# Performance work log

Measured on AMD Instinct MI355X. Metric: run time of the kernel, lower is better.

Reference implementation:

```python
import jax, jax.numpy as jnp
import numpy as np

B, N, E_PER = 64, 1024, 32768
IN_DIM, HID, K = 128, 128, 64
EPS = 1e-15


def setup_inputs() -> dict:
    key = jax.random.key(0)
    ks = jax.random.split(key, 16)
    x = jax.random.normal(ks[0], (B * N, IN_DIM), jnp.float32)
    off = (jnp.arange(B, dtype=jnp.int32) * N)[:, None]
    src = (jax.random.randint(ks[1], (B, E_PER), 0, N, dtype=jnp.int32) + off).reshape(-1)
    dst = (jax.random.randint(ks[2], (B, E_PER), 0, N, dtype=jnp.int32) + off).reshape(-1)
    edge_index = jnp.stack([src, dst])
    batch = jnp.repeat(jnp.arange(B, dtype=jnp.int32), N)

    def lin(k, i, o):
        return (jax.random.normal(k, (i, o), jnp.float32) / np.sqrt(i)).astype(jnp.float32)

    params = dict(
        W1l=lin(ks[3], IN_DIM, HID), b1l=jnp.zeros((HID,), jnp.float32), W1r=lin(ks[4], IN_DIM, HID),
        W2l=lin(ks[5], HID, K), b2l=jnp.zeros((K,), jnp.float32), W2r=lin(ks[6], HID, K),
        Wm=lin(ks[7], K, K), bm=jnp.zeros((K,), jnp.float32),
        Wrel=lin(ks[8], HID, HID), Wroot=lin(ks[9], HID, HID), broot=jnp.zeros((HID,), jnp.float32),
        Wc1=lin(ks[10], HID * K, HID), bc1=jnp.zeros((HID,), jnp.float32),
        Wc2=lin(ks[11], HID, 1), bc2=jnp.zeros((1,), jnp.float32),
    )
    return dict(x=x, edge_index=edge_index, batch=batch, num_graphs=B, nodes_per_graph=N, **params)


def _sage(x, src, dst, Wl, bl, Wr, n):
    # PyG SAGEConv: lin_l(mean_{j in N(i)} x_j) + lin_r(x_i); lin_r has no bias.
    agg = jax.ops.segment_sum(x[src], dst, num_segments=n)
    deg = jax.ops.segment_sum(jnp.ones((src.shape[0],), x.dtype), dst, num_segments=n)
    agg = agg / jnp.maximum(deg, 1.0)[:, None]
    return agg @ Wl + bl + x @ Wr


def reference(x, edge_index, batch, num_graphs, nodes_per_graph,
              W1l, b1l, W1r, W2l, b2l, W2r, Wm, bm,
              Wrel, Wroot, broot, Wc1, bc1, Wc2, bc2):
    Bn, Nn = num_graphs, nodes_per_graph
    n_total = Bn * Nn
    src, dst = edge_index[0], edge_index[1]

    z = jax.nn.leaky_relu(_sage(x, src, dst, W1l, b1l, W1r, n_total), 0.01)
    s = jax.nn.leaky_relu(_sage(z, src, dst, W2l, b2l, W2r, n_total), 0.01)
    s = s @ Wm + bm

    # to_dense_batch (equal-size graphs -> mask all True) and to_dense_adj
    z = z.reshape(Bn, Nn, -1)                      # [B, N, HID]
    s = s.reshape(Bn, Nn, -1)                      # [B, N, K]
    a = jnp.zeros((Bn, Nn, Nn), x.dtype).at[src // Nn, src % Nn, dst % Nn].add(1.0)

    # dense_diff_pool
    s = jax.nn.softmax(s, axis=-1)
    pooled = jnp.einsum('bnk,bnf->bkf', s, z)      # [B, K, HID]
    adj_p = jnp.einsum('bnk,bnm,bml->bkl', s, a, s)  # [B, K, K]
    link_loss = jnp.sqrt(jnp.sum((a - jnp.einsum('bnk,bmk->bnm', s, s)) ** 2)) / a.size
    ent_loss = jnp.mean(jnp.sum(-s * jnp.log(s + EPS), axis=-1))

    # DenseSAGEConv: lin_rel(adj@x / deg) + lin_root(x)
    agg = jnp.matmul(adj_p, pooled) / jnp.maximum(adj_p.sum(-1, keepdims=True), 1.0)
    h = jax.nn.leaky_relu(agg @ Wrel + pooled @ Wroot + broot, 0.01)

    h = h.reshape(Bn, -1)                          # [B, K*HID]
    logits = (jax.nn.leaky_relu(h @ Wc1 + bc1, 0.01) @ Wc2 + bc2).squeeze(-1)
    return logits, link_loss + ent_loss
```

## Files before the change

### kernel.cpp

```cpp
#include <hip/hip_runtime.h>
#include <math.h>

#define BATCH 64
#define NPG 1024
#define NT (BATCH*NPG)
#define EPER 32768
#define ETOT (BATCH*EPER)

typedef __attribute__((ext_vector_type(4))) float f32x4;
typedef __attribute__((ext_vector_type(8))) short s16x8;

__device__ __forceinline__ float lky(float x){ return x > 0.f ? x : 0.01f*x; }
__device__ __forceinline__ unsigned short f2bf(float f){
    unsigned u = __float_as_uint(f);
    u = u + 0x7FFFu + ((u >> 16) & 1u);
    return (unsigned short)(u >> 16);
}
__device__ __forceinline__ float bf2f_lo(unsigned v){ return __uint_as_float(v << 16); }
__device__ __forceinline__ float bf2f_hi(unsigned v){ return __uint_as_float(v & 0xFFFF0000u); }

__global__ void k_castx(const float* __restrict__ in, unsigned short* __restrict__ out, int n4){
    int i = blockIdx.x*256 + threadIdx.x;
    if (i < n4){
        float4 v = ((const float4*)in)[i];
        ushort4 o = { f2bf(v.x), f2bf(v.y), f2bf(v.z), f2bf(v.w) };
        ((ushort4*)out)[i] = o;
    }
}

__global__ void k_wprep(const float* __restrict__ W1l, const float* __restrict__ W1r,
                        const float* __restrict__ W2l, const float* __restrict__ W2r,
                        unsigned short* __restrict__ wt){
    int i = blockIdx.x*256 + threadIdx.x;
    if (i < 16384){ int k = i >> 7, n = i & 127; wt[n*128 + k] = f2bf(W1l[i]); }
    else if (i < 32768){ int j = i - 16384; int k = j >> 7, n = j & 127; wt[16384 + n*128 + k] = f2bf(W1r[j]); }
    else if (i < 40960){ int j = i - 32768; int k = j >> 6, n = j & 63; wt[32768 + n*128 + k] = f2bf(W2l[j]); }
    else if (i < 49152){ int j = i - 40960; int k = j >> 6, n = j & 63; wt[40960 + n*128 + k] = f2bf(W2r[j]); }
}

__global__ void __launch_bounds__(1024) k_a2lds(const int* __restrict__ src, const int* __restrict__ dst,
                                                unsigned* __restrict__ acc_out){
    __shared__ unsigned nib[32768];
    __shared__ unsigned red[16];
    int b = blockIdx.x, pass = blockIdx.y, tid = threadIdx.x;
    for (int i = tid; i < 32768; i += 1024) nib[i] = 0;
    __syncthreads();
    int base = b*EPER;
    for (int i = tid; i < EPER; i += 1024){
        unsigned key = (((unsigned)src[base+i] & 1023u) << 10) | ((unsigned)dst[base+i] & 1023u);
        if ((int)(key >> 18) == pass)
            atomicAdd(&nib[(key & 0x3FFFFu) >> 3], 1u << ((key & 7u)*4u));
    }
    __syncthreads();
    unsigned local = 0;
    for (int i = tid; i < 32768; i += 1024){
        unsigned w = nib[i];
        if (w){
            #pragma unroll
            for (int q = 0; q < 8; q++){ unsigned c = (w >> (4*q)) & 15u; local += c*c; }
        }
    }
    for (int o = 32; o; o >>= 1) local += __shfl_xor(local, o);
    if ((tid & 63) == 0) red[tid >> 6] = local;
    __syncthreads();
    if (tid == 0){
        unsigned s = 0;
        for (int q = 0; q < 16; q++) s += red[q];
        atomicAdd(acc_out, s);
    }
}

__global__ void __launch_bounds__(1024) k_csr(const int* __restrict__ src, const int* __restrict__ dst,
                                              int* __restrict__ ipd, int* __restrict__ ips,
                                              unsigned short* __restrict__ lst_d,
                                              unsigned short* __restrict__ lst_s){
    __shared__ unsigned eds[EPER];
    __shared__ int cnt[1024];
    __shared__ int buf[1024];
    int g = blockIdx.x, which = blockIdx.y, tid = threadIdx.x;
    cnt[tid] = 0;
    __syncthreads();
    int base = g*EPER;
    for (int i = tid; i < EPER; i += 1024){
        unsigned s = (unsigned)src[base+i] & 1023u;
        unsigned d = (unsigned)dst[base+i] & 1023u;
        eds[i] = (s << 10) | d;
        atomicAdd(&cnt[which ? s : d], 1);
    }
    __syncthreads();
    int v = cnt[tid];
    int x = v;
    buf[tid] = x; __syncthreads();
    for (int off = 1; off < 1024; off <<= 1){
        int t = (tid >= off) ? buf[tid - off] : 0;
        __syncthreads();
        x += t; buf[tid] = x; __syncthreads();
    }
    int excl = x - v;
    int* ip = which ? ips : ipd;
    ip[g*1024 + tid] = base + excl;
    if (g == 0 && tid == 0) ip[NT] = ETOT;
    cnt[tid] = excl;
    __syncthreads();
    unsigned short* lst = which ? lst_s : lst_d;
    for (int i = tid; i < EPER; i += 1024){
        unsigned key = eds[i];
        unsigned d = key & 1023u, s = key >> 10;
        unsigned idx = which ? s : d;
        unsigned val = which ? d : s;
        int p = atomicAdd(&cnt[idx], 1);
        lst[base + p] = (unsigned short)val;
    }
}

template<int MODE, int TD>
__global__ void __launch_bounds__(1024) k_aggl(
        const unsigned short* __restrict__ X, const int* __restrict__ indptr,
        const unsigned short* __restrict__ lst,
        const unsigned short* __restrict__ R, const float* __restrict__ bias,
        unsigned short* __restrict__ out){
    __shared__ uint2 tab[1024*9];
    constexpr int PPG = (TD == 128) ? 8 : 4;
    int bid = blockIdx.x;
    int xcd = bid & 7, j = bid >> 3;
    int gi = j / PPG, part = j - gi*PPG;
    int graph = xcd + 8*gi;
    int fpart = part >> 1;
    int npart = part & 1;
    int foff = fpart*32;
    int nbase_loc = npart*512;
    int tid = threadIdx.x;
    int gb = graph*NPG;
    for (int i = tid; i < 8192; i += 1024){
        int row = i >> 3, q = i & 7;
        tab[row*9 + q] = *(const uint2*)&X[(size_t)(gb+row)*TD + foff + q*4];
    }
    __syncthreads();
    int g = tid & 7;
    for (int c = 0; c < 4; c++){
        int node = gb + nbase_loc + c*128 + (tid >> 3);
        int st = indptr[node], en = indptr[node+1];
        float a0 = 0.f, a1 = 0.f, a2 = 0.f, a3 = 0.f;
        int e = st;
        for (; e + 4 <= en; e += 4){
            int r0 = lst[e+0], r1 = lst[e+1], r2 = lst[e+2], r3 = lst[e+3];
            uint2 v0 = tab[r0*9 + g];
            uint2 v1 = tab[r1*9 + g];
            uint2 v2 = tab[r2*9 + g];
            uint2 v3 = tab[r3*9 + g];
            a0 += bf2f_lo(v0.x) + bf2f_lo(v1.x) + bf2f_lo(v2.x) + bf2f_lo(v3.x);
            a1 += bf2f_hi(v0.x) + bf2f_hi(v1.x) + bf2f_hi(v2.x) + bf2f_hi(v3.x);
            a2 += bf2f_lo(v0.y) + bf2f_lo(v1.y) + bf2f_lo(v2.y) + bf2f_lo(v3.y);
            a3 += bf2f_hi(v0.y) + bf2f_hi(v1.y) + bf2f_hi(v2.y) + bf2f_hi(v3.y);
        }
        for (; e < en; e++){
            uint2 v = tab[lst[e]*9 + g];
            a0 += bf2f_lo(v.x); a1 += bf2f_hi(v.x);
            a2 += bf2f_lo(v.y); a3 += bf2f_hi(v.y);
        }
        if (MODE >= 1){
            int dg = en - st;
            float inv = 1.f/(float)(dg > 1 ? dg : 1);
            a0 *= inv; a1 *= inv; a2 *= inv; a3 *= inv;
        }
        if (MODE == 2){
            uint2 r = *(const uint2*)&R[(size_t)node*TD + foff + 4*g];
            a0 = lky(a0 + bf2f_lo(r.x) + bias[foff + 4*g + 0]);
            a1 = lky(a1 + bf2f_hi(r.x) + bias[foff + 4*g + 1]);
            a2 = lky(a2 + bf2f_lo(r.y) + bias[foff + 4*g + 2]);
            a3 = lky(a3 + bf2f_hi(r.y) + bias[foff + 4*g + 3]);
        }
        uint2 pk;
        pk.x = (unsigned)f2bf(a0) | ((unsigned)f2bf(a1) << 16);
        pk.y = (unsigned)f2bf(a2) | ((unsigned)f2bf(a3) << 16);
        *(uint2*)&out[(size_t)node*TD + foff + 4*g] = pk;
    }
}

template<int N>
__global__ void __launch_bounds__(512) k_mfma2b(
        const unsigned short* __restrict__ Ah, const unsigned short* __restrict__ Wt1,
        const unsigned short* __restrict__ Wt2, unsigned short* __restrict__ C1,
        unsigned short* __restrict__ C2){
    __shared__ unsigned short ldsB[2*N*128];
    int tid = threadIdx.x;
    for (int i = tid; i < N*64; i += 512){
        int n = i >> 6, kk = i & 63;
        int swz = (n*256 + 4*kk) ^ ((n & 7) << 4);
        *(unsigned*)((char*)ldsB + swz)         = ((const unsigned*)Wt1)[i];
        *(unsigned*)((char*)ldsB + N*256 + swz) = ((const unsigned*)Wt2)[i];
    }
    __syncthreads();
    int wave = tid >> 6, l = tid & 63;
    int lr = l & 15, lg = l >> 4;
    constexpr int NF = N/16;
    int arow = blockIdx.x*128 + wave*16 + lr;
    f32x4 acc1[NF], acc2[NF];
    f32x4 zv = {0.f, 0.f, 0.f, 0.f};
    #pragma unroll
    for (int nf = 0; nf < NF; nf++){ acc1[nf] = zv; acc2[nf] = zv; }
    #pragma unroll
    for (int ks = 0; ks < 4; ks++){
        s16x8 af = *(const s16x8*)(Ah + (size_t)arow*128 + ks*32 + lg*8);
        #pragma unroll
        for (int nf = 0; nf < NF; nf++){
            int n = nf*16 + lr;
            int swz = (n*256 + ks*64 + lg*16) ^ ((n & 7) << 4);
            s16x8 b1 = *(const s16x8*)((const char*)ldsB + swz);
            s16x8 b2 = *(const s16x8*)((const char*)ldsB + N*256 + swz);
            acc1[nf] = __builtin_amdgcn_mfma_f32_16x16x32_bf16(af, b1, acc1[nf], 0, 0, 0);
            acc2[nf] = __builtin_amdgcn_mfma_f32_16x16x32_bf16(af, b2, acc2[nf], 0, 0, 0);
        }
    }
    int orow = blockIdx.x*128 + wave*16 + lg*4;
    #pragma unroll
    for (int nf = 0; nf < NF; nf++){
        int c = nf*16 + lr;
        #pragma unroll
        for (int j = 0; j < 4; j++){
            size_t idx = (size_t)(orow + j)*N + c;
            C1[idx] = f2bf(acc1[nf][j]);
            C2[idx] = f2bf(acc2[nf][j]);
        }
    }
}

__global__ void __launch_bounds__(256) k_gemm(
        const float* __restrict__ A1, const float* __restrict__ A2,
        const float* __restrict__ W1, const float* __restrict__ W2,
        const float* __restrict__ bias, void* __restrict__ C,
        int M, int Nn, int Kd, int dual, int act, int obf){
    __shared__ float sA1[16*68], sB1[16*68], sA2[16*68], sB2[16*68];
    int tid = threadIdx.x;
    int m0 = blockIdx.x*64, n0 = blockIdx.y*64;
    int tx = tid & 15, ty = tid >> 4;
    int lr = tid >> 2, lk = (tid & 3)*4;
    int wk = tid >> 4, wn = (tid & 15)*4;
    float acc[4][4] = {};
    for (int k0 = 0; k0 < Kd; k0 += 16){
        float4 a1 = *(const float4*)&A1[(size_t)(m0+lr)*Kd + k0 + lk];
        float4 w1 = *(const float4*)&W1[(size_t)(k0+wk)*Nn + n0 + wn];
        sA1[(lk+0)*68+lr] = a1.x; sA1[(lk+1)*68+lr] = a1.y;
        sA1[(lk+2)*68+lr] = a1.z; sA1[(lk+3)*68+lr] = a1.w;
        *(float4*)&sB1[wk*68+wn] = w1;
        if (dual){
            float4 a2 = *(const float4*)&A2[(size_t)(m0+lr)*Kd + k0 + lk];
            float4 w2 = *(const float4*)&W2[(size_t)(k0+wk)*Nn + n0 + wn];
            sA2[(lk+0)*68+lr] = a2.x; sA2[(lk+1)*68+lr] = a2.y;
            sA2[(lk+2)*68+lr] = a2.z; sA2[(lk+3)*68+lr] = a2.w;
            *(float4*)&sB2[wk*68+wn] = w2;
        }
        __syncthreads();
        #pragma unroll
        for (int kk = 0; kk < 16; kk++){
            float4 av = *(const float4*)&sA1[kk*68 + ty*4];
            float4 bv = *(const float4*)&sB1[kk*68 + tx*4];
            float a[4] = {av.x, av.y, av.z, av.w};
            float b[4] = {bv.x, bv.y, bv.z, bv.w};
            #pragma unroll
            for (int i = 0; i < 4; i++)
                #pragma unroll
                for (int j = 0; j < 4; j++) acc[i][j] += a[i]*b[j];
            if (dual){
                float4 av2 = *(const float4*)&sA2[kk*68 + ty*4];
                float4 bv2 = *(const float4*)&sB2[kk*68 + tx*4];
                float a2[4] = {av2.x, av2.y, av2.z, av2.w};
                float b2[4] = {bv2.x, bv2.y, bv2.z, bv2.w};
                #pragma unroll
                for (int i = 0; i < 4; i++)
                    #pragma unroll
                    for (int j = 0; j < 4; j++) acc[i][j] += a2[i]*b2[j];
            }
        }
        __syncthreads();
    }
    float bb[4] = {0.f, 0.f, 0.f, 0.f};
    if (bias){
        #pragma unroll
        for (int j = 0; j < 4; j++) bb[j] = bias[n0 + tx*4 + j];
    }
    #pragma unroll
    for (int i = 0; i < 4; i++){
        float v0 = acc[i][0]+bb[0], v1 = acc[i][1]+bb[1], v2 = acc[i][2]+bb[2], v3 = acc[i][3]+bb[3];
        if (act){ v0 = lky(v0); v1 = lky(v1); v2 = lky(v2); v3 = lky(v3); }
        size_t idx = (size_t)(m0 + ty*4 + i)*Nn + n0 + tx*4;
        if (obf){
            ushort4 o = { f2bf(v0), f2bf(v1), f2bf(v2), f2bf(v3) };
            *(ushort4*)&((unsigned short*)C)[idx] = o;
        } else {
            float4 o = { v0, v1, v2, v3 };
            *(float4*)&((float*)C)[idx] = o;
        }
    }
}

__global__ void __launch_bounds__(256) k_gemm_wm(
        const unsigned short* __restrict__ agg2h, const unsigned short* __restrict__ r2h,
        const float* __restrict__ b2l, const float* __restrict__ Wm,
        const float* __restrict__ bm,
        unsigned short* __restrict__ Sh, float* __restrict__ ent_acc){
    __shared__ float sA[16*68], sB[16*68];
    __shared__ float red[256];
    int tid = threadIdx.x;
    int m0 = blockIdx.x*64;
    int tx = tid & 15, ty = tid >> 4;
    int lr = tid >> 2, lk = (tid & 3)*4;
    int wk = tid >> 4, wn = (tid & 15)*4;
    float acc[4][4] = {};
    for (int k0 = 0; k0 < 64; k0 += 16){
        uint2 a = *(const uint2*)&agg2h[(size_t)(m0+lr)*64 + k0 + lk];
        uint2 r = *(const uint2*)&r2h[(size_t)(m0+lr)*64 + k0 + lk];
        sA[(lk+0)*68+lr] = lky(bf2f_lo(a.x) + bf2f_lo(r.x) + b2l[k0+lk+0]);
        sA[(lk+1)*68+lr] = lky(bf2f_hi(a.x) + bf2f_hi(r.x) + b2l[k0+lk+1]);
        sA[(lk+2)*68+lr] = lky(bf2f_lo(a.y) + bf2f_lo(r.y) + b2l[k0+lk+2]);
        sA[(lk+3)*68+lr] = lky(bf2f_hi(a.y) + bf2f_hi(r.y) + b2l[k0+lk+3]);
        *(float4*)&sB[wk*68+wn] = *(const float4*)&Wm[(size_t)(k0+wk)*64 + wn];
        __syncthreads();
        #pragma unroll
        for (int kk = 0; kk < 16; kk++){
            float4 av = *(const float4*)&sA[kk*68 + ty*4];
            float4 bv = *(const float4*)&sB[kk*68 + tx*4];
            float a4[4] = {av.x, av.y, av.z, av.w};
            float b4[4] = {bv.x, bv.y, bv.z, bv.w};
            #pragma unroll
            for (int i = 0; i < 4; i++)
                #pragma unroll
                for (int j = 0; j < 4; j++) acc[i][j] += a4[i]*b4[j];
        }
        __syncthreads();
    }
    float bb[4];
    #pragma unroll
    for (int j = 0; j < 4; j++) bb[j] = bm[tx*4 + j];
    float ent_local = 0.f;
    #pragma unroll
    for (int i = 0; i < 4; i++){
        float v[4];
        #pragma unroll
        for (int j = 0; j < 4; j++) v[j] = acc[i][j] + bb[j];
        float m = fmaxf(fmaxf(v[0], v[1]), fmaxf(v[2], v[3]));
        for (int o = 1; o < 16; o <<= 1) m = fmaxf(m, __shfl_xor(m, o));
        float e[4];
        float sm = 0.f;
        #pragma unroll
        for (int j = 0; j < 4; j++){ e[j] = __expf(v[j] - m); sm += e[j]; }
        for (int o = 1; o < 16; o <<= 1) sm += __shfl_xor(sm, o);
        float inv = 1.f/sm;
        float p[4];
        float w = 0.f;
        #pragma unroll
        for (int j = 0; j < 4; j++){
            p[j] = e[j]*inv;
            w += -p[j]*__logf(p[j] + 1e-15f);
        }
        for (int o = 1; o < 16; o <<= 1) w += __shfl_xor(w, o);
        if (tx == 0) ent_local += w;
        size_t idx = (size_t)(m0 + ty*4 + i)*64 + tx*4;
        ushort4 oh = { f2bf(p[0]), f2bf(p[1]), f2bf(p[2]), f2bf(p[3]) };
        *(ushort4*)&Sh[idx] = oh;
    }
    red[tid] = ent_local; __syncthreads();
    for (int o = 128; o; o >>= 1){ if (tid < o) red[tid] += red[tid+o]; __syncthreads(); }
    if (tid == 0) atomicAdd(ent_acc, red[0]);
}

__global__ void __launch_bounds__(1024) k_spmm(
        const unsigned short* __restrict__ Sh, const unsigned short* __restrict__ Zh,
        const unsigned short* __restrict__ Th, float* __restrict__ pbuf){
    __shared__ unsigned short At[64*72];
    __shared__ unsigned short Bt[256*72];
    int bid = blockIdx.x;
    int xcd = bid & 7, j = bid >> 3;
    int graph = xcd + 8*(j & 7);
    int kp = j >> 3;
    int tid = threadIdx.x;
    int w = tid >> 6, l = tid & 63;
    int lr = l & 15, lg = l >> 4;
    int mt = w & 3, ng = w >> 2;
    f32x4 acc[4];
    f32x4 zv = {0.f, 0.f, 0.f, 0.f};
    #pragma unroll
    for (int q = 0; q < 4; q++) acc[q] = zv;
    int gb = graph*NPG;
    int sa_n = tid & 63, sa_c = (tid >> 6)*4;
    int sb_k = tid & 63, sb_g = tid >> 6;
    for (int n0 = kp*256; n0 < kp*256 + 256; n0 += 64){
        ushort4 sv = *(const ushort4*)&Sh[(size_t)(gb+n0+sa_n)*64 + sa_c];
        At[(sa_c+0)*72 + sa_n] = sv.x;
        At[(sa_c+1)*72 + sa_n] = sv.y;
        At[(sa_c+2)*72 + sa_n] = sv.z;
        At[(sa_c+3)*72 + sa_n] = sv.w;
        {
            int R = gb + n0 + sb_k;
            const unsigned short* srcp;
            if (sb_g < 8)       srcp = &Zh[(size_t)R*128 + sb_g*16];
            else if (sb_g < 12) srcp = &Th[(size_t)R*64 + (sb_g-8)*16];
            else                srcp = &Sh[(size_t)R*64 + (sb_g-12)*16];
            ushort4 a0 = *(const ushort4*)(srcp);
            ushort4 a1 = *(const ushort4*)(srcp+4);
            ushort4 a2 = *(const ushort4*)(srcp+8);
            ushort4 a3 = *(const ushort4*)(srcp+12);
            int cb = sb_g*16;
            Bt[(cb+ 0)*72+sb_k]=a0.x; Bt[(cb+ 1)*72+sb_k]=a0.y; Bt[(cb+ 2)*72+sb_k]=a0.z; Bt[(cb+ 3)*72+sb_k]=a0.w;
            Bt[(cb+ 4)*72+sb_k]=a1.x; Bt[(cb+ 5)*72+sb_k]=a1.y; Bt[(cb+ 6)*72+sb_k]=a1.z; Bt[(cb+ 7)*72+sb_k]=a1.w;
            Bt[(cb+ 8)*72+sb_k]=a2.x; Bt[(cb+ 9)*72+sb_k]=a2.y; Bt[(cb+10)*72+sb_k]=a2.z; Bt[(cb+11)*72+sb_k]=a2.w;
            Bt[(cb+12)*72+sb_k]=a3.x; Bt[(cb+13)*72+sb_k]=a3.y; Bt[(cb+14)*72+sb_k]=a3.z; Bt[(cb+15)*72+sb_k]=a3.w;
        }
        __syncthreads();
        #pragma unroll
        for (int ks = 0; ks < 2; ks++){
            s16x8 af = *(const s16x8*)&At[(mt*16+lr)*72 + ks*32 + lg*8];
            #pragma unroll
            for (int q = 0; q < 4; q++){
                s16x8 bf = *(const s16x8*)&Bt[((ng*4+q)*16+lr)*72 + ks*32 + lg*8];
                acc[q] = __builtin_amdgcn_mfma_f32_16x16x32_bf16(af, bf, acc[q], 0, 0, 0);
            }
        }
        __syncthreads();
    }
    float* pb = pbuf + ((size_t)graph*4 + kp)*16384;
    #pragma unroll
    for (int q = 0; q < 4; q++){
        int col = (ng*4+q)*16 + lr;
        #pragma unroll
        for (int j2 = 0; j2 < 4; j2++){
            int m = mt*16 + lg*4 + j2;
            pb[m*256 + col] = acc[q][j2];
        }
    }
}

__global__ void k_spmmred(const float* __restrict__ pbuf,
                          float* __restrict__ P, float* __restrict__ AP,
                          float* __restrict__ GR,
                          float* __restrict__ redt, float* __restrict__ reds){
    int i = blockIdx.x*256 + threadIdx.x;
    int g = i >> 14;
    int r = i & 16383;
    int m = r >> 8, col = r & 255;
    const float* pb = pbuf + (size_t)g*65536 + r;
    float v = pb[0] + pb[16384] + pb[32768] + pb[49152];
    float tr = 0.f, sq = 0.f;
    if (col < 128){
        P[((size_t)g*64 + m)*128 + col] = v;
    } else if (col < 192){
        AP[((size_t)g*64 + m)*64 + (col-128)] = v;
        if (col-128 == m) tr = v;
    } else {
        GR[((size_t)g*64 + m)*64 + (col-192)] = v;
        sq = v*v;
    }
    for (int o = 32; o; o >>= 1){ tr += __shfl_xor(tr, o); sq += __shfl_xor(sq, o); }
    __shared__ float rt[4], rs[4];
    if ((threadIdx.x & 63) == 0){ rt[threadIdx.x >> 6] = tr; rs[threadIdx.x >> 6] = sq; }
    __syncthreads();
    if (threadIdx.x == 0){
        redt[blockIdx.x] = rt[0]+rt[1]+rt[2]+rt[3];
        reds[blockIdx.x] = rs[0]+rs[1]+rs[2]+rs[3];
    }
}

__global__ void __launch_bounds__(1024) k_redfin(const float* __restrict__ redt,
                                                 const float* __restrict__ reds,
                                                 float* __restrict__ crossp,
                                                 float* __restrict__ normgp){
    int tid = threadIdx.x;
    float t = redt[tid] + redt[tid+1024] + redt[tid+2048] + redt[tid+3072];
    float s = reds[tid] + reds[tid+1024] + reds[tid+2048] + reds[tid+3072];
    for (int o = 32; o; o >>= 1){ t += __shfl_xor(t, o); s += __shfl_xor(s, o); }
    __shared__ float rt[16], rs[16];
    if ((tid & 63) == 0){ rt[tid >> 6] = t; rs[tid >> 6] = s; }
    __syncthreads();
    if (tid == 0){
        float st = 0.f, ss = 0.f;
        for (int q = 0; q < 16; q++){ st += rt[q]; ss += rs[q]; }
        atomicAdd(crossp, st);
        atomicAdd(normgp, ss);
    }
}

__global__ void __launch_bounds__(256) k_heada(
        const float* __restrict__ AP, const float* __restrict__ P,
        float* __restrict__ aggout){
    __shared__ float sapT[64*65];
    __shared__ float sp[64*33];
    __shared__ float srs[64];
    int b = blockIdx.x, c0 = blockIdx.y*32;
    int tid = threadIdx.x;
    for (int i = tid; i < 4096; i += 256){
        int k = i >> 6, l = i & 63;
        sapT[l*65 + k] = AP[(size_t)b*4096 + i];
    }
    for (int i = tid; i < 2048; i += 256){
        int l = i >> 5, j = i & 31;
        sp[l*33 + j] = P[(size_t)b*8192 + l*128 + c0 + j];
    }
    __syncthreads();
    if (tid < 64){
        float s = 0.f;
        for (int l = 0; l < 64; l++) s += sapT[l*65 + tid];
        srs[tid] = fmaxf(s, 1.f);
    }
    __syncthreads();
    int k = tid & 63, jg = (tid >> 6)*8;
    float acc[8] = {};
    for (int l = 0; l < 64; l++){
        float a = sapT[l*65 + k];
        #pragma unroll
        for (int j = 0; j < 8; j++) acc[j] += a*sp[l*33 + jg + j];
    }
    float inv = 1.f/srs[k];
    #pragma unroll
    for (int j = 0; j < 8; j++)
        aggout[(size_t)b*8192 + k*128 + c0 + jg + j] = acc[j]*inv;
}

__global__ void __launch_bounds__(256) k_head2(
        const float* __restrict__ hbuf, const float* __restrict__ Wc1,
        float* __restrict__ hcacc){
    __shared__ float sh[512];
    __shared__ float sred[256];
    int b = blockIdx.x >> 4, ch = blockIdx.x & 15;
    int tid = threadIdx.x;
    for (int i = tid; i < 512; i += 256) sh[i] = hbuf[(size_t)b*8192 + ch*512 + i];
    __syncthreads();
    int j = tid & 127, half = tid >> 7;
    float acc = 0.f;
    const float* W = Wc1 + (size_t)(ch*512 + half*256)*128;
    const float* hh = sh + half*256;
    for (int r = 0; r < 256; r++) acc += hh[r]*W[(size_t)r*128 + j];
    sred[tid] = acc; __syncthreads();
    if (tid < 128) atomicAdd(&hcacc[(size_t)b*128 + tid], sred[tid] + sred[tid+128]);
}

__global__ void k_head3(const float* __restrict__ hcacc, const float* __restrict__ bc1,
                        const float* __restrict__ Wc2, const float* __restrict__ bc2,
                        float* __restrict__ out){
    int b = blockIdx.x, t = threadIdx.x;
    float hc = lky(hcacc[(size_t)b*128 + t] + bc1[t]);
    float p = hc*Wc2[t];
    for (int o = 32; o; o >>= 1) p += __shfl_xor(p, o);
    __shared__ float r2[2];
    if ((t & 63) == 0) r2[t >> 6] = p;
    __syncthreads();
    if (t == 0) out[b] = r2[0] + r2[1] + bc2[0];
}

__global__ void k_finalize(const unsigned int* __restrict__ a2,
                           const float* __restrict__ cross,
                           const float* __restrict__ normg,
                           const float* __restrict__ ent,
                           float* __restrict__ out){
    float ss = (float)(*a2) - 2.f*(*cross) + (*normg);
    if (ss < 0.f) ss = 0.f;
    float link = sqrtf(ss) / 67108864.f;
    out[64] = link + (*ent)/(float)NT;
}

extern "C" void kernel_launch(void* const* d_in, const int* in_sizes, int n_in,
                              void* d_out, int out_size, void* d_ws, size_t ws_size,
                              hipStream_t stream){
    const float* x    = (const float*)d_in[0];
    const int*   ei   = (const int*)d_in[1];
    const int*   src  = ei;
    const int*   dst  = ei + ETOT;
    const float* W1l  = (const float*)d_in[5];
    const float* b1l  = (const float*)d_in[6];
    const float* W1r  = (const float*)d_in[7];
    const float* W2l  = (const float*)d_in[8];
    const float* b2l  = (const float*)d_in[9];
    const float* W2r  = (const float*)d_in[10];
    const float* Wm   = (const float*)d_in[11];
    const float* bm   = (const float*)d_in[12];
    const float* Wrel = (const float*)d_in[13];
    const float* Wroot= (const float*)d_in[14];
    const float* broot= (const float*)d_in[15];
    const float* Wc1  = (const float*)d_in[16];
    const float* bc1  = (const float*)d_in[17];
    const float* Wc2  = (const float*)d_in[18];
    const float* bc2  = (const float*)d_in[19];
    float* out = (float*)d_out;

    char* w = (char*)d_ws;
    size_t off = 0;
    auto take = [&](size_t bytes)->void*{
        void* p = w + off; off = (off + bytes + 255) & ~(size_t)255; return p;
    };
    const size_t MB = 1024*1024;
    float* hcacc  = (float*)take((size_t)BATCH*128*4);
    float* accb   = (float*)take(64);
    size_t zero_small = off;
    unsigned short* wt = (unsigned short*)take((size_t)49152*2);
    float* pooled = (float*)take((size_t)BATCH*64*128*4);
    float* adjp   = (float*)take((size_t)BATCH*64*64*4);
    float* gram   = (float*)take((size_t)BATCH*64*64*4);
    float* redt   = (float*)take((size_t)4096*4);
    float* reds   = (float*)take((size_t)4096*4);
    int*   ipd   = (int*)take((size_t)(NT+1)*4);
    int*   ips   = (int*)take((size_t)(NT+1)*4);
    unsigned short* lst_d = (unsigned short*)take((size_t)ETOT*2);
    unsigned short* lst_s = (unsigned short*)take((size_t)ETOT*2);
    char*  regA  = (char*)take(16*MB);
    char*  regB  = (char*)take(16*MB);
    char*  regC  = (char*)take(16*MB);
    char*  regD  = (char*)take(16*MB);
    char*  regE  = (char*)take(16*MB);
    float* hbuf  = (float*)take((size_t)BATCH*8192*4);
    float* aggo  = (float*)take((size_t)BATCH*8192*4);

    unsigned short* y1h   = (unsigned short*)regB;
    unsigned short* th    = (unsigned short*)regB;
    unsigned short* r1h   = (unsigned short*)regC;
    unsigned short* y2h   = (unsigned short*)regC;
    unsigned short* s2h   = (unsigned short*)(regC + 8*MB);
    unsigned short* r2h   = (unsigned short*)regD;
    float*          pbuf  = (float*)regD;
    unsigned short* xh    = (unsigned short*)regE;
    unsigned short* zh    = (unsigned short*)regE;
    unsigned short* agg2h = (unsigned short*)regA;

    float* crossp = accb + 0;
    float* normgp = accb + 1;
    float* entp   = accb + 2;
    unsigned int* a2p = (unsigned int*)(accb + 3);

    hipMemsetAsync(d_ws, 0, zero_small, stream);

    k_wprep<<<192, 256, 0, stream>>>(W1l, W1r, W2l, W2r, wt);
    k_castx<<<NT*128/4/256, 256, 0, stream>>>(x, xh, NT*128/4);

    k_a2lds<<<dim3(BATCH, 4), 1024, 0, stream>>>(src, dst, a2p);

    k_csr<<<dim3(BATCH, 2), 1024, 0, stream>>>(src, dst, ipd, ips, lst_d, lst_s);

    k_mfma2b<128><<<NT/128, 512, 0, stream>>>(xh, wt, wt + 16384, y1h, r1h);
    k_aggl<2,128><<<512, 1024, 0, stream>>>(y1h, ipd, lst_d, r1h, b1l, zh);

    k_mfma2b<64><<<NT/128, 512, 0, stream>>>(zh, wt + 32768, wt + 40960, y2h, r2h);
    k_aggl<1,64><<<256, 1024, 0, stream>>>(y2h, ipd, lst_d, nullptr, nullptr, agg2h);
    k_gemm_wm<<<NT/64, 256, 0, stream>>>(agg2h, r2h, b2l, Wm, bm, s2h, entp);

    k_aggl<0,64><<<256, 1024, 0, stream>>>(s2h, ips, lst_s, nullptr, nullptr, th);

    k_spmm<<<256, 1024, 0, stream>>>(s2h, zh, th, pbuf);
    k_spmmred<<<4096, 256, 0, stream>>>(pbuf, pooled, adjp, gram, redt, reds);
    k_redfin<<<1, 1024, 0, stream>>>(redt, reds, crossp, normgp);

    k_heada<<<dim3(BATCH, 4), 256, 0, stream>>>(adjp, pooled, aggo);
    k_gemm<<<dim3(BATCH*64/64, 2), 256, 0, stream>>>(aggo, pooled, Wrel, Wroot, broot, hbuf, BATCH*64, 128, 128, 1, 1, 0);
    k_head2<<<BATCH*16, 256, 0, stream>>>(hbuf, Wc1, hcacc);
    k_head3<<<BATCH, 128, 0, stream>>>(hcacc, bc1, Wc2, bc2, out);
    k_finalize<<<1, 1, 0, stream>>>(a2p, crossp, normgp, entp, out);
}
```

Measured before the change: 267.5 us.

## Compute adjacency squared-norm from CSR duplicate pairs instead of LDS nibble histogram

Drops the separate histogram kernel that rebuilt each graph's dense adjacency as 4-bit counters in shared memory over four passes. The sum of squared edge multiplicities is now derived as edge count plus twice the number of duplicate (src,dst) pairs, counted per destination node from the already-built CSR lists. The two CSR builds per graph are merged into one block that reuses the staged edge array. This cuts one full pass over the edge list and the big shared-memory allocation, at the cost of a quadratic per-node duplicate scan and one block per graph doing two serial sorts.

```diff
diff --git a/kernel.cpp b/kernel.cpp
--- a/kernel.cpp
+++ b/kernel.cpp
@@ -6,6 +6,7 @@
 #define NT (BATCH*NPG)
 #define EPER 32768
 #define ETOT (BATCH*EPER)
+#define DCAP 10240
 
 typedef __attribute__((ext_vector_type(4))) float f32x4;
 typedef __attribute__((ext_vector_type(8))) short s16x8;
@@ -38,78 +39,116 @@
     else if (i < 49152){ int j = i - 40960; int k = j >> 6, n = j & 63; wt[40960 + n*128 + k] = f2bf(W2r[j]); }
 }
 
-__global__ void __launch_bounds__(1024) k_a2lds(const int* __restrict__ src, const int* __restrict__ dst,
-                                                unsigned* __restrict__ acc_out){
-    __shared__ unsigned nib[32768];
-    __shared__ unsigned red[16];
-    int b = blockIdx.x, pass = blockIdx.y, tid = threadIdx.x;
-    for (int i = tid; i < 32768; i += 1024) nib[i] = 0;
-    __syncthreads();
-    int base = b*EPER;
-    for (int i = tid; i < EPER; i += 1024){
-        unsigned key = (((unsigned)src[base+i] & 1023u) << 10) | ((unsigned)dst[base+i] & 1023u);
-        if ((int)(key >> 18) == pass)
-            atomicAdd(&nib[(key & 0x3FFFFu) >> 3], 1u << ((key & 7u)*4u));
-    }
-    __syncthreads();
-    unsigned local = 0;
-    for (int i = tid; i < 32768; i += 1024){
-        unsigned w = nib[i];
-        if (w){
-            #pragma unroll
-            for (int q = 0; q < 8; q++){ unsigned c = (w >> (4*q)) & 15u; local += c*c; }
-        }
-    }
-    for (int o = 32; o; o >>= 1) local += __shfl_xor(local, o);
-    if ((tid & 63) == 0) red[tid >> 6] = local;
-    __syncthreads();
-    if (tid == 0){
-        unsigned s = 0;
-        for (int q = 0; q < 16; q++) s += red[q];
-        atomicAdd(acc_out, s);
-    }
-}
-
-__global__ void __launch_bounds__(1024) k_csr(const int* __restrict__ src, const int* __restrict__ dst,
-                                              int* __restrict__ ipd, int* __restrict__ ips,
-                                              unsigned short* __restrict__ lst_d,
-                                              unsigned short* __restrict__ lst_s){
+__global__ void __launch_bounds__(1024) k_csr2(const int* __restrict__ src, const int* __restrict__ dst,
+                                               int* __restrict__ ipd, int* __restrict__ ips,
+                                               unsigned short* __restrict__ lst_d,
+                                               unsigned short* __restrict__ lst_s){
     __shared__ unsigned eds[EPER];
     __shared__ int cnt[1024];
     __shared__ int buf[1024];
-    int g = blockIdx.x, which = blockIdx.y, tid = threadIdx.x;
+    int g = blockIdx.x, tid = threadIdx.x;
+    int base = g*EPER;
     cnt[tid] = 0;
     __syncthreads();
-    int base = g*EPER;
     for (int i = tid; i < EPER; i += 1024){
         unsigned s = (unsigned)src[base+i] & 1023u;
         unsigned d = (unsigned)dst[base+i] & 1023u;
         eds[i] = (s << 10) | d;
-        atomicAdd(&cnt[which ? s : d], 1);
-    }
-    __syncthreads();
-    int v = cnt[tid];
-    int x = v;
-    buf[tid] = x; __syncthreads();
-    for (int off = 1; off < 1024; off <<= 1){
-        int t = (tid >= off) ? buf[tid - off] : 0;
-        __syncthreads();
-        x += t; buf[tid] = x; __syncthreads();
-    }
-    int excl = x - v;
-    int* ip = which ? ips : ipd;
-    ip[g*1024 + tid] = base + excl;
-    if (g == 0 && tid == 0) ip[NT] = ETOT;
-    cnt[tid] = excl;
-    __syncthreads();
-    unsigned short* lst = which ? lst_s : lst_d;
-    for (int i = tid; i < EPER; i += 1024){
-        unsigned key = eds[i];
-        unsigned d = key & 1023u, s = key >> 10;
-        unsigned idx = which ? s : d;
-        unsigned val = which ? d : s;
-        int p = atomicAdd(&cnt[idx], 1);
-        lst[base + p] = (unsigned short)val;
+        atomicAdd(&cnt[d], 1);
+    }
+    __syncthreads();
+    {
+        int v = cnt[tid];
+        int x = v;
+        buf[tid] = x; __syncthreads();
+        for (int off = 1; off < 1024; off <<= 1){
+            int t = (tid >= off) ? buf[tid - off] : 0;
+            __syncthreads();
+            x += t; buf[tid] = x; __syncthreads();
+        }
+        int excl = x - v;
+        ipd[g*1024 + tid] = base + excl;
+        if (g == 0 && tid == 0) ipd[NT] = ETOT;
+        cnt[tid] = excl;
+        __syncthreads();
+        for (int i = tid; i < EPER; i += 1024){
+            unsigned key = eds[i];
+            unsigned d = key & 1023u, s = key >> 10;
+            int p = atomicAdd(&cnt[d], 1);
+            lst_d[base + p] = (unsigned short)s;
+        }
+    }
+    __syncthreads();
+    cnt[tid] = 0;
+    __syncthreads();
+    for (int i = tid; i < EPER; i += 1024) atomicAdd(&cnt[eds[i] >> 10], 1);
+    __syncthreads();
+    {
+        int v = cnt[tid];
+        int x = v;
+        buf[tid] = x; __syncthreads();
+        for (int off = 1; off < 1024; off <<= 1){
+            int t = (tid >= off) ? buf[tid - off] : 0;
+            __syncthreads();
+            x += t; buf[tid] = x; __syncthreads();
+        }
+        int excl = x - v;
+        ips[g*1024 + tid] = base + excl;
+        if (g == 0 && tid == 0) ips[NT] = ETOT;
+        cnt[tid] = excl;
+        __syncthreads();
+        for (int i = tid; i < EPER; i += 1024){
+            unsigned key = eds[i];
+            unsigned d = key & 1023u, s = key >> 10;
+            int p = atomicAdd(&cnt[s], 1);
+            lst_s[base + p] = (unsigned short)d;
+        }
+    }
+}
+
+__global__ void __launch_bounds__(1024) k_dup(const int* __restrict__ ipd,
+                                              const unsigned short* __restrict__ lst_d,
+                                              unsigned* __restrict__ pairs_out){
+    __shared__ unsigned short elds[DCAP];
+    __shared__ unsigned red[16];
+    int bid = blockIdx.x;
+    int xcd = bid & 7, j = bid >> 3;
+    int gi = j >> 2, part = j & 3;
+    int graph = xcd + 8*gi;
+    int gb = graph*NPG;
+    int tid = threadIdx.x;
+    int estart = ipd[gb + part*256];
+    int eend   = ipd[gb + part*256 + 256];
+    int ecount = eend - estart;
+    bool staged = (ecount <= DCAP);
+    if (staged){
+        for (int i = tid; i < ecount; i += 1024) elds[i] = lst_d[estart + i];
+    }
+    __syncthreads();
+    int node = part*256 + (tid >> 2);
+    int sub = tid & 3;
+    int st = ipd[gb + node] - estart;
+    int en = ipd[gb + node + 1] - estart;
+    unsigned local = 0;
+    if (staged){
+        for (int i = st + sub; i < en; i += 4){
+            unsigned short v = elds[i];
+            for (int jj = i + 1; jj < en; jj++) local += (elds[jj] == v);
+        }
+    } else {
+        const unsigned short* gl = lst_d + estart;
+        for (int i = st + sub; i < en; i += 4){
+            unsigned short v = gl[i];
+            for (int jj = i + 1; jj < en; jj++) local += (gl[jj] == v);
+        }
+    }
+    for (int o = 32; o; o >>= 1) local += __shfl_xor(local, o);
+    if ((tid & 63) == 0) red[tid >> 6] = local;
+    __syncthreads();
+    if (tid == 0){
+        unsigned s = 0;
+        for (int q = 0; q < 16; q++) s += red[q];
+        atomicAdd(pairs_out, s);
     }
 }
 
@@ -546,12 +585,13 @@
     if (t == 0) out[b] = r2[0] + r2[1] + bc2[0];
 }
 
-__global__ void k_finalize(const unsigned int* __restrict__ a2,
+__global__ void k_finalize(const unsigned int* __restrict__ pairs,
                            const float* __restrict__ cross,
                            const float* __restrict__ normg,
                            const float* __restrict__ ent,
                            float* __restrict__ out){
-    float ss = (float)(*a2) - 2.f*(*cross) + (*normg);
+    float a2 = (float)ETOT + 2.f*(float)(*pairs);
+    float ss = a2 - 2.f*(*cross) + (*normg);
     if (ss < 0.f) ss = 0.f;
     float link = sqrtf(ss) / 67108864.f;
     out[64] = link + (*ent)/(float)NT;
@@ -622,16 +662,15 @@
     float* crossp = accb + 0;
     float* normgp = accb + 1;
     float* entp   = accb + 2;
-    unsigned int* a2p = (unsigned int*)(accb + 3);
+    unsigned int* pairsp = (unsigned int*)(accb + 3);
 
     hipMemsetAsync(d_ws, 0, zero_small, stream);
 
     k_wprep<<<192, 256, 0, stream>>>(W1l, W1r, W2l, W2r, wt);
     k_castx<<<NT*128/4/256, 256, 0, stream>>>(x, xh, NT*128/4);
 
-    k_a2lds<<<dim3(BATCH, 4), 1024, 0, stream>>>(src, dst, a2p);
-
-    k_csr<<<dim3(BATCH, 2), 1024, 0, stream>>>(src, dst, ipd, ips, lst_d, lst_s);
+    k_csr2<<<BATCH, 1024, 0, stream>>>(src, dst, ipd, ips, lst_d, lst_s);
+    k_dup<<<256, 1024, 0, stream>>>(ipd, lst_d, pairsp);
 
     k_mfma2b<128><<<NT/128, 512, 0, stream>>>(xh, wt, wt + 16384, y1h, r1h);
     k_aggl<2,128><<<512, 1024, 0, stream>>>(y1h, ipd, lst_d, r1h, b1l, zh);
@@ -650,5 +689,5 @@
     k_gemm<<<dim3(BATCH*64/64, 2), 256, 0, stream>>>(aggo, pooled, Wrel, Wroot, broot, hbuf, BATCH*64, 128, 128, 1, 1, 0);
     k_head2<<<BATCH*16, 256, 0, stream>>>(hbuf, Wc1, hcacc);
     k_head3<<<BATCH, 128, 0, stream>>>(hcacc, bc1, Wc2, bc2, out);
-    k_finalize<<<1, 1, 0, stream>>>(a2p, crossp, normgp, entp, out);
-}
+    k_finalize<<<1, 1, 0, stream>>>(pairsp, crossp, normgp, entp, out);
+}
```

After: 302.8 us. 1.13x slower.

## Fold sum of squared adjacency counts into CSR build via duplicate-pair counting

Applied to the files above, without the earlier changes.

Drops the separate k_a2lds kernel, which built a nibble histogram of the dense adjacency in LDS to get sum(a^2). The CSR kernel now scatters each destination's source list into an LDS staging buffer and counts duplicate pairs per row, using sum(c^2) = E + 2*pairs. The CSR list is then copied out with 16-byte vector stores instead of scattered 2-byte global writes. The per-row duplicate count is quadratic in degree and uneven across threads, but degrees here are small (about 32).

```diff
diff --git a/kernel.cpp b/kernel.cpp
--- a/kernel.cpp
+++ b/kernel.cpp
@@ -38,55 +38,23 @@
     else if (i < 49152){ int j = i - 40960; int k = j >> 6, n = j & 63; wt[40960 + n*128 + k] = f2bf(W2r[j]); }
 }
 
-__global__ void __launch_bounds__(1024) k_a2lds(const int* __restrict__ src, const int* __restrict__ dst,
-                                                unsigned* __restrict__ acc_out){
-    __shared__ unsigned nib[32768];
-    __shared__ unsigned red[16];
-    int b = blockIdx.x, pass = blockIdx.y, tid = threadIdx.x;
-    for (int i = tid; i < 32768; i += 1024) nib[i] = 0;
-    __syncthreads();
-    int base = b*EPER;
-    for (int i = tid; i < EPER; i += 1024){
-        unsigned key = (((unsigned)src[base+i] & 1023u) << 10) | ((unsigned)dst[base+i] & 1023u);
-        if ((int)(key >> 18) == pass)
-            atomicAdd(&nib[(key & 0x3FFFFu) >> 3], 1u << ((key & 7u)*4u));
-    }
-    __syncthreads();
-    unsigned local = 0;
-    for (int i = tid; i < 32768; i += 1024){
-        unsigned w = nib[i];
-        if (w){
-            #pragma unroll
-            for (int q = 0; q < 8; q++){ unsigned c = (w >> (4*q)) & 15u; local += c*c; }
-        }
-    }
-    for (int o = 32; o; o >>= 1) local += __shfl_xor(local, o);
-    if ((tid & 63) == 0) red[tid >> 6] = local;
-    __syncthreads();
-    if (tid == 0){
-        unsigned s = 0;
-        for (int q = 0; q < 16; q++) s += red[q];
-        atomicAdd(acc_out, s);
-    }
-}
-
 __global__ void __launch_bounds__(1024) k_csr(const int* __restrict__ src, const int* __restrict__ dst,
                                               int* __restrict__ ipd, int* __restrict__ ips,
                                               unsigned short* __restrict__ lst_d,
-                                              unsigned short* __restrict__ lst_s){
-    __shared__ unsigned eds[EPER];
+                                              unsigned short* __restrict__ lst_s,
+                                              unsigned* __restrict__ pairs_out){
+    __shared__ unsigned short stage[EPER];
     __shared__ int cnt[1024];
     __shared__ int buf[1024];
+    __shared__ unsigned redp[16];
     int g = blockIdx.x, which = blockIdx.y, tid = threadIdx.x;
+    int base = g*EPER;
     cnt[tid] = 0;
     __syncthreads();
-    int base = g*EPER;
-    for (int i = tid; i < EPER; i += 1024){
-        unsigned s = (unsigned)src[base+i] & 1023u;
-        unsigned d = (unsigned)dst[base+i] & 1023u;
-        eds[i] = (s << 10) | d;
-        atomicAdd(&cnt[which ? s : d], 1);
-    }
+    const int* keyarr = which ? src : dst;
+    const int* valarr = which ? dst : src;
+    for (int i = tid; i < EPER; i += 1024)
+        atomicAdd(&cnt[keyarr[base+i] & 1023], 1);
     __syncthreads();
     int v = cnt[tid];
     int x = v;
@@ -102,14 +70,31 @@
     if (g == 0 && tid == 0) ip[NT] = ETOT;
     cnt[tid] = excl;
     __syncthreads();
+    for (int i = tid; i < EPER; i += 1024){
+        int k = keyarr[base+i] & 1023;
+        int val = valarr[base+i] & 1023;
+        int p = atomicAdd(&cnt[k], 1);
+        stage[p] = (unsigned short)val;
+    }
+    __syncthreads();
     unsigned short* lst = which ? lst_s : lst_d;
-    for (int i = tid; i < EPER; i += 1024){
-        unsigned key = eds[i];
-        unsigned d = key & 1023u, s = key >> 10;
-        unsigned idx = which ? s : d;
-        unsigned val = which ? d : s;
-        int p = atomicAdd(&cnt[idx], 1);
-        lst[base + p] = (unsigned short)val;
+    for (int i = tid; i < EPER/8; i += 1024)
+        ((uint4*)(lst + base))[i] = ((const uint4*)stage)[i];
+    if (which == 0){
+        unsigned local = 0;
+        int st = excl, en = excl + v;
+        for (int i = st; i < en; i++){
+            unsigned short vv = stage[i];
+            for (int jj = i + 1; jj < en; jj++) local += (stage[jj] == vv);
+        }
+        for (int o = 32; o; o >>= 1) local += __shfl_xor(local, o);
+        if ((tid & 63) == 0) redp[tid >> 6] = local;
+        __syncthreads();
+        if (tid == 0){
+            unsigned s = 0;
+            for (int q = 0; q < 16; q++) s += redp[q];
+            atomicAdd(pairs_out, s);
+        }
     }
 }
 
@@ -546,12 +531,13 @@
     if (t == 0) out[b] = r2[0] + r2[1] + bc2[0];
 }
 
-__global__ void k_finalize(const unsigned int* __restrict__ a2,
+__global__ void k_finalize(const unsigned int* __restrict__ pairs,
                            const float* __restrict__ cross,
                            const float* __restrict__ normg,
                            const float* __restrict__ ent,
                            float* __restrict__ out){
-    float ss = (float)(*a2) - 2.f*(*cross) + (*normg);
+    float a2 = (float)ETOT + 2.f*(float)(*pairs);
+    float ss = a2 - 2.f*(*cross) + (*normg);
     if (ss < 0.f) ss = 0.f;
     float link = sqrtf(ss) / 67108864.f;
     out[64] = link + (*ent)/(float)NT;
@@ -622,16 +608,14 @@
     float* crossp = accb + 0;
     float* normgp = accb + 1;
     float* entp   = accb + 2;
-    unsigned int* a2p = (unsigned int*)(accb + 3);
+    unsigned int* pairsp = (unsigned int*)(accb + 3);
 
     hipMemsetAsync(d_ws, 0, zero_small, stream);
 
     k_wprep<<<192, 256, 0, stream>>>(W1l, W1r, W2l, W2r, wt);
     k_castx<<<NT*128/4/256, 256, 0, stream>>>(x, xh, NT*128/4);
 
-    k_a2lds<<<dim3(BATCH, 4), 1024, 0, stream>>>(src, dst, a2p);
-
-    k_csr<<<dim3(BATCH, 2), 1024, 0, stream>>>(src, dst, ipd, ips, lst_d, lst_s);
+    k_csr<<<dim3(BATCH, 2), 1024, 0, stream>>>(src, dst, ipd, ips, lst_d, lst_s, pairsp);
 
     k_mfma2b<128><<<NT/128, 512, 0, stream>>>(xh, wt, wt + 16384, y1h, r1h);
     k_aggl<2,128><<<512, 1024, 0, stream>>>(y1h, ipd, lst_d, r1h, b1l, zh);
@@ -650,5 +634,5 @@
     k_gemm<<<dim3(BATCH*64/64, 2), 256, 0, stream>>>(aggo, pooled, Wrel, Wroot, broot, hbuf, BATCH*64, 128, 128, 1, 1, 0);
     k_head2<<<BATCH*16, 256, 0, stream>>>(hbuf, Wc1, hcacc);
     k_head3<<<BATCH, 128, 0, stream>>>(hcacc, bc1, Wc2, bc2, out);
-    k_finalize<<<1, 1, 0, stream>>>(a2p, crossp, normgp, entp, out);
-}
+    k_finalize<<<1, 1, 0, stream>>>(pairsp, crossp, normgp, entp, out);
+}
```

New measurement: 312.9 us. 17.0% more time.
